# Optimization experiments

Measured on AMD Instinct MI355X. Metric: run time of the kernel, lower is better.

The kernel has to match this reference:

```python
import jax, jax.numpy as jnp
import numpy as np
from jax import lax

B, H, W, CIN = 4, 64, 64, 1024
CMID = 512
NA = 9  # 3 sizes * 3 ratios
PRE_NMS, POST_NMS, IOU_THR = 6000, 300, 0.7  # eval-mode caps (training=False)


def setup_inputs() -> dict:
    key = jax.random.key(0)
    ks = jax.random.split(key, 4)
    feats = jax.random.normal(ks[0], (B, H, W, CIN), jnp.float32)
    # anchors: normalized ccwh (cx, cy, w, h) on a stride-16 grid of a 1024px image
    stride, img = 16.0, 1024.0
    cx = (jnp.arange(W, dtype=jnp.float32) + 0.5) * stride / img
    cy = (jnp.arange(H, dtype=jnp.float32) + 0.5) * stride / img
    sizes = jnp.array([64.0, 128.0, 256.0])
    ratios = jnp.array([0.5, 1.0, 2.0])
    ws = (sizes[:, None] * jnp.sqrt(ratios)[None, :]).reshape(-1) / img  # [9]
    hs = (sizes[:, None] / jnp.sqrt(ratios)[None, :]).reshape(-1) / img  # [9]
    cyg, cxg = jnp.meshgrid(cy, cx, indexing='ij')  # [H,W]
    ancs = jnp.stack([
        jnp.broadcast_to(cxg[:, :, None], (H, W, NA)),
        jnp.broadcast_to(cyg[:, :, None], (H, W, NA)),
        jnp.broadcast_to(ws[None, None, :], (H, W, NA)),
        jnp.broadcast_to(hs[None, None, :], (H, W, NA)),
    ], axis=-1)
    ancs = jnp.broadcast_to(ancs[None], (B, H, W, NA, 4)).astype(jnp.float32)
    ancs_valid = jnp.ones((B, H, W, NA), jnp.float32)
    w_bneck = jax.random.normal(ks[1], (CIN, CMID), jnp.float32) * 0.01
    b_bneck = jnp.zeros((CMID,), jnp.float32)
    w_cls = jax.random.normal(ks[2], (CMID, NA), jnp.float32) * 0.01
    b_cls = jnp.zeros((NA,), jnp.float32)
    w_reg = jax.random.normal(ks[3], (CMID, NA * 4), jnp.float32) * 0.01
    b_reg = jnp.zeros((NA * 4,), jnp.float32)
    return dict(feats=feats, ancs=ancs, ancs_valid=ancs_valid,
                w_bneck=w_bneck, b_bneck=b_bneck, w_cls=w_cls, b_cls=b_cls,
                w_reg=w_reg, b_reg=b_reg)


def _nms(boxes, max_out, thr):
    # boxes [N,4] xyxy, sorted by score descending. Greedy NMS via lax.scan.
    x1, y1, x2, y2 = boxes[:, 0], boxes[:, 1], boxes[:, 2], boxes[:, 3]
    areas = (x2 - x1) * (y2 - y1)

    def step(valid, _):
        idx = jnp.argmax(valid)  # first still-valid box = highest score
        has = valid[idx]
        b = boxes[idx]
        a = areas[idx]
        iw = jnp.maximum(jnp.minimum(b[2], x2) - jnp.maximum(b[0], x1), 0.0)
        ih = jnp.maximum(jnp.minimum(b[3], y2) - jnp.maximum(b[1], y1), 0.0)
        inter = iw * ih
        union = a + areas - inter
        iou = jnp.where(union > 0, inter / union, 0.0)
        keep = valid & (iou <= thr)
        keep = keep.at[idx].set(False)
        return jnp.where(has, keep, valid), jnp.where(has, idx, -1)

    _, sel = lax.scan(step, jnp.ones(boxes.shape[0], bool), None, length=max_out)
    return sel  # [max_out] selected indices, -1 = no more boxes


def _forward(feats, ancs, w_bneck, b_bneck, w_cls, b_cls, w_reg, b_reg):
    h = jax.nn.relu(jnp.einsum('bhwc,cm->bhwm', feats, w_bneck) + b_bneck)
    cls_pred = jax.nn.sigmoid(jnp.einsum('bhwm,mo->bhwo', h, w_cls) + b_cls)
    reg_pred = (jnp.einsum('bhwm,mo->bhwo', h, w_reg) + b_reg).reshape(B, H, W, NA, 4)
    cls_f = cls_pred.reshape(-1)
    reg_f = reg_pred.reshape(-1, 4)
    anc_f = ancs.reshape(-1, 4)
    # apply_offsets in ccwh: cx += tx*w, cy += ty*h, w *= exp(tw), h *= exp(th)
    cx = anc_f[:, 0] + reg_f[:, 0] * anc_f[:, 2]
    cy = anc_f[:, 1] + reg_f[:, 1] * anc_f[:, 3]
    ww = anc_f[:, 2] * jnp.exp(reg_f[:, 2])
    hh = anc_f[:, 3] * jnp.exp(reg_f[:, 3])
    # ccwh -> xyxy, clip to [0,1]
    boxes = jnp.stack([cx - ww / 2, cy - hh / 2, cx + ww / 2, cy + hh / 2], axis=-1)
    boxes = jnp.clip(boxes, 0.0, 1.0)
    order = jnp.argsort(-cls_f)[:PRE_NMS]
    boxes = boxes[order]
    sel = _nms(boxes, POST_NMS, IOU_THR)
    # pad unselected slots with zeros (TF returns a variable-length tensor)
    proposals = jnp.where(sel[:, None] >= 0, boxes[jnp.clip(sel, 0)], 0.0)
    return cls_pred, reg_pred, proposals


def reference(feats, ancs, ancs_valid, w_bneck, b_bneck, w_cls, b_cls, w_reg, b_reg):
    # ancs_valid is reshaped but never used in the original extract_proposals
    return _forward(feats, ancs, w_bneck, b_bneck, w_cls, b_cls, w_reg, b_reg)
```

## Files before the change

kernel.cpp:

```cpp
#include <hip/hip_runtime.h>
#include <cstdint>
#include <cstddef>

#define P_TOT    16384
#define CIN      1024
#define CMID     512
#define NA       9
#define NANC     147456
#define PRE_NMS  6000
#define POST_NMS 300
#define IOU_THR  0.7f
#define NWORDS   94
#define NHCOPY   64

#define CLS_OFF  0
#define REG_OFF  147456
#define PROP_OFF 737280

#define WS_H        0u
#define WS_MASK     0u
#define WS_HISTN    8388608u
#define WS_LOGITS   33554432u
#define WS_BOXES    36700160u
#define WS_HIST     39059456u
#define WS_WCOMB    39059456u
#define WS_META     39321600u
#define WS_COLL     39321856u
#define WS_SBOX     39387392u
#define CAP_COLL    8192

__device__ __forceinline__ int imin(int a, int b) { return a < b ? a : b; }

__device__ __forceinline__ void gld_lds16(const float* g, float* l) {
    __builtin_amdgcn_global_load_lds(
        (const __attribute__((address_space(1))) void*)g,
        (__attribute__((address_space(3))) void*)l,
        16, 0, 0);
}

__global__ __launch_bounds__(256)
__attribute__((amdgpu_waves_per_eu(1, 2)))
void gemm1_kernel(
    const float* __restrict__ A, const float* __restrict__ Bw,
    const float* __restrict__ bias, float* __restrict__ C)
{
    __shared__ float As[2][16][132];
    __shared__ float Bs[2][16][128];

    const int t  = threadIdx.x;
    const int m0 = blockIdx.x * 128;
    const int n0 = blockIdx.y * 128;
    const int tx = t & 15;
    const int ty = t >> 4;

    const int ar0 = t >> 2;
    const int ac0 = (t & 3) * 4;

    const float* asrc0 = A + (size_t)(m0 + ar0) * CIN + ac0;
    const float* asrc1 = asrc0 + (size_t)64 * CIN;
    const float* bsrc  = Bw + (size_t)(t >> 5) * CMID + n0 + (t & 31) * 4;
    float* bdst0 = &Bs[0][0][0] + t * 4;
    float* bdst1 = &Bs[1][0][0] + t * 4;

    float4 c0a{0,0,0,0}, c0b{0,0,0,0}, c1a{0,0,0,0}, c1b{0,0,0,0};
    float4 c2a{0,0,0,0}, c2b{0,0,0,0}, c3a{0,0,0,0}, c3b{0,0,0,0};
    float4 c4a{0,0,0,0}, c4b{0,0,0,0}, c5a{0,0,0,0}, c5b{0,0,0,0};
    float4 c6a{0,0,0,0}, c6b{0,0,0,0}, c7a{0,0,0,0}, c7b{0,0,0,0};

    gld_lds16(bsrc, bdst0);
    gld_lds16(bsrc + 8 * CMID, bdst0 + 1024);
    float4 pa0 = *(const float4*)(asrc0);
    float4 pa1 = *(const float4*)(asrc1);
    As[0][ac0 + 0][ar0] = pa0.x; As[0][ac0 + 1][ar0] = pa0.y;
    As[0][ac0 + 2][ar0] = pa0.z; As[0][ac0 + 3][ar0] = pa0.w;
    As[0][ac0 + 0][ar0 + 64] = pa1.x; As[0][ac0 + 1][ar0 + 64] = pa1.y;
    As[0][ac0 + 2][ar0 + 64] = pa1.z; As[0][ac0 + 3][ar0 + 64] = pa1.w;
    __syncthreads();

#define FMA4(acc, s, b) { acc.x += (s)*(b).x; acc.y += (s)*(b).y; \
                          acc.z += (s)*(b).z; acc.w += (s)*(b).w; }

    for (int kt = 0; kt < 64; ++kt) {
        const int cur = kt & 1, nxt = cur ^ 1;
        if (kt < 63) {
            const int k0 = (kt + 1) * 16;
            float* bd = nxt ? bdst1 : bdst0;
            gld_lds16(bsrc + (size_t)k0 * CMID, bd);
            gld_lds16(bsrc + (size_t)(k0 + 8) * CMID, bd + 1024);
            pa0 = *(const float4*)(asrc0 + k0);
            pa1 = *(const float4*)(asrc1 + k0);
        }
#pragma unroll 2
        for (int kk = 0; kk < 16; ++kk) {
            float4 a0 = *(const float4*)&As[cur][kk][ty * 4];
            float4 a1 = *(const float4*)&As[cur][kk][64 + ty * 4];
            float4 b0 = *(const float4*)&Bs[cur][kk][tx * 4];
            float4 b1 = *(const float4*)&Bs[cur][kk][64 + tx * 4];
            FMA4(c0a, a0.x, b0) FMA4(c0b, a0.x, b1)
            FMA4(c1a, a0.y, b0) FMA4(c1b, a0.y, b1)
            FMA4(c2a, a0.z, b0) FMA4(c2b, a0.z, b1)
            FMA4(c3a, a0.w, b0) FMA4(c3b, a0.w, b1)
            FMA4(c4a, a1.x, b0) FMA4(c4b, a1.x, b1)
            FMA4(c5a, a1.y, b0) FMA4(c5b, a1.y, b1)
            FMA4(c6a, a1.z, b0) FMA4(c6b, a1.z, b1)
            FMA4(c7a, a1.w, b0) FMA4(c7b, a1.w, b1)
        }
        if (kt < 63) {
            As[nxt][ac0 + 0][ar0] = pa0.x; As[nxt][ac0 + 1][ar0] = pa0.y;
            As[nxt][ac0 + 2][ar0] = pa0.z; As[nxt][ac0 + 3][ar0] = pa0.w;
            As[nxt][ac0 + 0][ar0 + 64] = pa1.x; As[nxt][ac0 + 1][ar0 + 64] = pa1.y;
            As[nxt][ac0 + 2][ar0 + 64] = pa1.z; As[nxt][ac0 + 3][ar0 + 64] = pa1.w;
        }
        __syncthreads();
    }
#undef FMA4

    const float4 bias0 = *(const float4*)(bias + n0 + tx * 4);
    const float4 bias1 = *(const float4*)(bias + n0 + 64 + tx * 4);
#define STROW(row, ca, cb) { \
    float4 o; \
    o.x = fmaxf(ca.x + bias0.x, 0.f); o.y = fmaxf(ca.y + bias0.y, 0.f); \
    o.z = fmaxf(ca.z + bias0.z, 0.f); o.w = fmaxf(ca.w + bias0.w, 0.f); \
    *(float4*)(C + (size_t)(row) * CMID + n0 + tx * 4) = o; \
    o.x = fmaxf(cb.x + bias1.x, 0.f); o.y = fmaxf(cb.y + bias1.y, 0.f); \
    o.z = fmaxf(cb.z + bias1.z, 0.f); o.w = fmaxf(cb.w + bias1.w, 0.f); \
    *(float4*)(C + (size_t)(row) * CMID + n0 + 64 + tx * 4) = o; }

    const int mr = m0 + ty * 4;
    STROW(mr + 0, c0a, c0b)   STROW(mr + 1, c1a, c1b)
    STROW(mr + 2, c2a, c2b)   STROW(mr + 3, c3a, c3b)
    STROW(mr + 64, c4a, c4b)  STROW(mr + 65, c5a, c5b)
    STROW(mr + 66, c6a, c6b)  STROW(mr + 67, c7a, c7b)
#undef STROW
}

__global__ __launch_bounds__(256) void wprep_kernel(
    const float* __restrict__ wcls, const float* __restrict__ wreg,
    float* __restrict__ wcomb)
{
    int i = blockIdx.x * 256 + threadIdx.x;
    int k = i / 48, o = i - k * 48;
    float v = 0.f;
    if (o < 9)       v = wcls[k * 9 + o];
    else if (o < 45) v = wreg[k * 36 + (o - 9)];
    wcomb[i] = v;
}

__global__ __launch_bounds__(256) void gemm2_kernel(
    const float* __restrict__ h, const float* __restrict__ wcomb,
    const float* __restrict__ bcls, const float* __restrict__ breg,
    float* __restrict__ logits)
{
    __shared__ float hS[64][33];
    __shared__ float wS[32][48];

    const int t  = threadIdx.x;
    const int p0 = blockIdx.x * 64;
    const int px = t & 63;
    const int og = t >> 6;

    const int hr = t >> 2;
    const int hc = (t & 3) * 4;

    float acc[12] = {};

    for (int kt = 0; kt < 16; ++kt) {
        const int k0 = kt * 32;
        {
            const float* hp = h + (size_t)(p0 + hr) * CMID + k0 + hc;
            float4 v0 = *(const float4*)(hp);
            float4 v1 = *(const float4*)(hp + 16);
            hS[hr][hc + 0] = v0.x; hS[hr][hc + 1] = v0.y;
            hS[hr][hc + 2] = v0.z; hS[hr][hc + 3] = v0.w;
            hS[hr][16 + hc + 0] = v1.x; hS[hr][16 + hc + 1] = v1.y;
            hS[hr][16 + hc + 2] = v1.z; hS[hr][16 + hc + 3] = v1.w;
        }
        {
            int idx = t;
            if (idx < 384) {
                int kk = idx / 12, o4 = (idx - kk * 12) * 4;
                *(float4*)&wS[kk][o4] = *(const float4*)&wcomb[(size_t)(k0 + kk) * 48 + o4];
            }
            idx = t + 256;
            if (idx < 384) {
                int kk = idx / 12, o4 = (idx - kk * 12) * 4;
                *(float4*)&wS[kk][o4] = *(const float4*)&wcomb[(size_t)(k0 + kk) * 48 + o4];
            }
        }
        __syncthreads();
#pragma unroll 4
        for (int kk = 0; kk < 32; ++kk) {
            float hv = hS[px][kk];
            float4 w0 = *(const float4*)&wS[kk][og * 12];
            float4 w1 = *(const float4*)&wS[kk][og * 12 + 4];
            float4 w2 = *(const float4*)&wS[kk][og * 12 + 8];
            acc[0] += hv * w0.x; acc[1]  += hv * w0.y; acc[2]  += hv * w0.z; acc[3]  += hv * w0.w;
            acc[4] += hv * w1.x; acc[5]  += hv * w1.y; acc[6]  += hv * w1.z; acc[7]  += hv * w1.w;
            acc[8] += hv * w2.x; acc[9]  += hv * w2.y; acc[10] += hv * w2.z; acc[11] += hv * w2.w;
        }
        __syncthreads();
    }
#pragma unroll
    for (int c = 0; c < 12; ++c) {
        int o = og * 12 + c;
        if (o < 45) {
            float bv = (o < 9) ? bcls[o] : breg[o - 9];
            logits[(size_t)(p0 + px) * 48 + o] = acc[c] + bv;
        }
    }
}

__global__ __launch_bounds__(256) void decode_kernel(
    const float* __restrict__ logits, const float4* __restrict__ ancs,
    float* __restrict__ out, float4* __restrict__ boxes,
    unsigned int* __restrict__ histN)
{
    int i = blockIdx.x * 256 + threadIdx.x;
    int p = i / 9, a = i - p * 9;
    const float* lrow = logits + (size_t)p * 48;
    float lg = lrow[a];
    float score = 1.f / (1.f + expf(-lg));
    out[CLS_OFF + i] = score;

    float r0 = lrow[9 + a * 4 + 0];
    float r1 = lrow[9 + a * 4 + 1];
    float r2 = lrow[9 + a * 4 + 2];
    float r3 = lrow[9 + a * 4 + 3];
    float4 rg; rg.x = r0; rg.y = r1; rg.z = r2; rg.w = r3;
    *(float4*)(out + REG_OFF + (size_t)i * 4) = rg;

    float4 an = ancs[i];
    float cx = an.x + r0 * an.z;
    float cy = an.y + r1 * an.w;
    float ww = an.z * expf(r2);
    float hh = an.w * expf(r3);
    float4 bb;
    bb.x = fminf(fmaxf(cx - ww * 0.5f, 0.f), 1.f);
    bb.y = fminf(fmaxf(cy - hh * 0.5f, 0.f), 1.f);
    bb.z = fminf(fmaxf(cx + ww * 0.5f, 0.f), 1.f);
    bb.w = fminf(fmaxf(cy + hh * 0.5f, 0.f), 1.f);
    boxes[i] = bb;

    unsigned int sb = __float_as_uint(score);
    atomicAdd(&histN[(unsigned)(blockIdx.x & (NHCOPY - 1)) * 65536u + (sb >> 16)], 1u);
}

__global__ __launch_bounds__(256) void hreduce_kernel(
    const unsigned int* __restrict__ histN, unsigned int* __restrict__ hist)
{
    int b = blockIdx.x * 256 + threadIdx.x;
    unsigned int s = 0;
#pragma unroll 8
    for (int c = 0; c < NHCOPY; ++c) s += histN[(unsigned)c * 65536u + b];
    hist[b] = s;
}

__global__ __launch_bounds__(256) void scan_kernel(
    const unsigned int* __restrict__ hist, unsigned int* __restrict__ meta)
{
    __shared__ unsigned int sums[256];
    __shared__ unsigned int sc[256];
    __shared__ unsigned int sc2[256];
    __shared__ int cstar;
    __shared__ unsigned int saShared;
    __shared__ int tbin;

    int t = threadIdx.x;
    if (t == 0) tbin = -1;

    unsigned int s = 0;
    int base = t << 8;
    for (int b = 0; b < 256; b += 4) {
        uint4 v = *(const uint4*)(hist + base + b);
        s += v.x + v.y + v.z + v.w;
    }
    sums[t] = s;
    __syncthreads();

    sc[t] = sums[255 - t];
    __syncthreads();
    for (int off = 1; off < 256; off <<= 1) {
        unsigned int v = sc[t];
        unsigned int add = (t >= off) ? sc[t - off] : 0u;
        __syncthreads();
        sc[t] = v + add;
        __syncthreads();
    }
    {
        unsigned int sa = (t == 255) ? 0u : sc[254 - t];
        if (sa < PRE_NMS && sa + sums[t] >= PRE_NMS) { cstar = t; saShared = sa; }
    }
    __syncthreads();

    int c = cstar;
    unsigned int SA = saShared;
    sc2[t] = hist[c * 256 + 255 - t];
    __syncthreads();
    for (int off = 1; off < 256; off <<= 1) {
        unsigned int v = sc2[t];
        unsigned int add = (t >= off) ? sc2[t - off] : 0u;
        __syncthreads();
        sc2[t] = v + add;
        __syncthreads();
    }
    {
        unsigned int si = sc2[255 - t];
        int cand = (SA + si >= PRE_NMS) ? t : -1;
        atomicMax(&tbin, cand);
    }
    __syncthreads();
    if (t == 0) meta[1] = (unsigned int)(c * 256 + tbin);
}

__global__ __launch_bounds__(256) void collect_kernel(
    const float* __restrict__ scores, const unsigned int* __restrict__ meta,
    unsigned long long* __restrict__ coll, unsigned int* __restrict__ cnt)
{
    int i = blockIdx.x * 256 + threadIdx.x;
    unsigned int T = meta[1];
    unsigned int sb = __float_as_uint(scores[i]);
    if ((sb >> 16) >= T) {
        unsigned int pos = atomicAdd(cnt, 1u);
        if (pos < CAP_COLL)
            coll[pos] = ((unsigned long long)sb << 32) |
                        (unsigned long long)(0xFFFFFFFFu - (unsigned int)i);
    }
}

__global__ __launch_bounds__(256) void rank_kernel(
    const unsigned long long* __restrict__ coll,
    const unsigned int* __restrict__ cnt,
    const float4* __restrict__ boxes, float4* __restrict__ sboxes)
{
    const int t = threadIdx.x;
    const int lane = t & 63;
    const int gwave = blockIdx.x * 4 + (t >> 6);
    unsigned int n = cnt[0];
    if (n > CAP_COLL) n = CAP_COLL;
    if (gwave * 16 >= (int)n) return;

    unsigned long long me[16];
    int rank[16];
#pragma unroll
    for (int i = 0; i < 16; ++i) {
        int mi = gwave * 16 + i;
        me[i] = (mi < (int)n) ? coll[mi] : ~0ULL;
        rank[i] = 0;
    }

    for (int j = 0; j < CAP_COLL; j += 64) {
        unsigned long long k = ((unsigned)(j + lane) < n) ? coll[j + lane] : 0ULL;
#pragma unroll
        for (int i = 0; i < 16; ++i)
            rank[i] += (int)__popcll(__ballot(k > me[i]));
    }

#pragma unroll
    for (int i = 0; i < 16; ++i) {
        int mi = gwave * 16 + i;
        if (mi < (int)n && rank[i] < PRE_NMS && lane == i) {
            unsigned int idx = 0xFFFFFFFFu - (unsigned int)(me[i] & 0xFFFFFFFFULL);
            if (idx > NANC - 1) idx = NANC - 1;
            sboxes[rank[i]] = boxes[idx];
        }
    }
}

__global__ __launch_bounds__(64) void nmsmat_kernel(
    const float4* __restrict__ sboxes, unsigned long long* __restrict__ mask)
{
    const int rb = blockIdx.x, cb = blockIdx.y;
    if (cb < rb) return;
    __shared__ float cx1[64], cy1[64], cx2[64], cy2[64], car[64];

    const int t = threadIdx.x;
    const int c = cb * 64 + t;
    float4 b = (c < PRE_NMS) ? sboxes[c] : make_float4(0.f, 0.f, 0.f, 0.f);
    cx1[t] = b.x; cy1[t] = b.y; cx2[t] = b.z; cy2[t] = b.w;
    car[t] = (b.z - b.x) * (b.w - b.y);
    __syncthreads();

    const int r = rb * 64 + t;
    if (r >= PRE_NMS) return;
    const float4 rbx = sboxes[r];
    const float ra = (rbx.z - rbx.x) * (rbx.w - rbx.y);

    unsigned long long w = 0ULL;
#pragma unroll 8
    for (int i = 0; i < 64; ++i) {
        int j = cb * 64 + i;
        float iw = fmaxf(fminf(rbx.z, cx2[i]) - fmaxf(rbx.x, cx1[i]), 0.f);
        float ih = fmaxf(fminf(rbx.w, cy2[i]) - fmaxf(rbx.y, cy1[i]), 0.f);
        float inter = iw * ih;
        float uni = ra + car[i] - inter;
        float iou = (uni > 0.f) ? (inter / uni) : 0.f;
        if (iou > IOU_THR && j > r) w |= (1ULL << i);
    }
    mask[(size_t)r * NWORDS + cb] = w;
}

__global__ __launch_bounds__(64) void nmsresolve_kernel(
    const float4* __restrict__ sboxes,
    const unsigned long long* __restrict__ mask,
    float* __restrict__ prop)
{
    const int t = threadIdx.x;
    for (int j = t; j < POST_NMS * 4; j += 64) prop[j] = 0.f;

    const int w0 = 2 * t, w1 = 2 * t + 1;
    unsigned long long v0 = 0ULL, v1 = 0ULL;
    if (w0 < 93) v0 = ~0ULL; else if (w0 == 93) v0 = (1ULL << 48) - 1ULL;
    if (w1 < 93) v1 = ~0ULL; else if (w1 == 93) v1 = (1ULL << 48) - 1ULL;

    int cnt = 0;
    while (cnt < POST_NMS) {
        int c = 0x7fffffff;
        if (v0) c = (w0 << 6) + __builtin_ctzll(v0);
        else if (v1) c = (w1 << 6) + __builtin_ctzll(v1);
        unsigned long long bal = __ballot((v0 | v1) != 0ULL);
        if (!bal) break;
        int F = __builtin_ctzll(bal);
        int g = __shfl(c, F, 64);
        const int wg = g >> 6, bg = g & 63;

        if (t == 0) {
            float4 bb = sboxes[g];
            *(float4*)(prop + cnt * 4) = bb;
        }
        unsigned long long mx = 0ULL, my = 0ULL;
        if (t < 47) {
            const ulonglong2* row2 = (const ulonglong2*)(mask + (size_t)g * NWORDS);
            ulonglong2 mm = row2[t];
            mx = mm.x; my = mm.y;
        }
        unsigned long long m0 = (w0 >= wg) ? mx : 0ULL;
        unsigned long long m1 = (w1 >= wg) ? my : 0ULL;
        v0 &= ~m0; v1 &= ~m1;
        if (w0 == wg) v0 &= ~(1ULL << bg);
        if (w1 == wg) v1 &= ~(1ULL << bg);
        ++cnt;
    }
}

extern "C" void kernel_launch(void* const* d_in, const int* in_sizes, int n_in,
                              void* d_out, int out_size, void* d_ws, size_t ws_size,
                              hipStream_t stream)
{
    const float*  feats   = (const float*)d_in[0];
    const float4* ancs    = (const float4*)d_in[1];
    const float*  w_bneck = (const float*)d_in[3];
    const float*  b_bneck = (const float*)d_in[4];
    const float*  w_cls   = (const float*)d_in[5];
    const float*  b_cls   = (const float*)d_in[6];
    const float*  w_reg   = (const float*)d_in[7];
    const float*  b_reg   = (const float*)d_in[8];

    float* out = (float*)d_out;
    char*  ws  = (char*)d_ws;
    float*              h      = (float*)(ws + WS_H);
    float*              logits = (float*)(ws + WS_LOGITS);
    float4*             boxes  = (float4*)(ws + WS_BOXES);
    unsigned int*       histN  = (unsigned int*)(ws + WS_HISTN);
    unsigned int*       hist   = (unsigned int*)(ws + WS_HIST);
    float*              wcomb  = (float*)(ws + WS_WCOMB);
    unsigned int*       meta   = (unsigned int*)(ws + WS_META);
    unsigned long long* coll   = (unsigned long long*)(ws + WS_COLL);
    float4*             sboxes = (float4*)(ws + WS_SBOX);
    unsigned long long* mask   = (unsigned long long*)(ws + WS_MASK);

    hipMemsetAsync(ws + WS_META, 0, 256, stream);

    wprep_kernel<<<96, 256, 0, stream>>>(w_cls, w_reg, wcomb);
    gemm1_kernel<<<dim3(128, 4), 256, 0, stream>>>(feats, w_bneck, b_bneck, h);
    gemm2_kernel<<<256, 256, 0, stream>>>(h, wcomb, b_cls, b_reg, logits);
    hipMemsetAsync(ws + WS_HISTN, 0, (size_t)NHCOPY * 65536 * 4, stream);
    decode_kernel<<<576, 256, 0, stream>>>(logits, ancs, out, boxes, histN);
    hreduce_kernel<<<256, 256, 0, stream>>>(histN, hist);
    scan_kernel<<<1, 256, 0, stream>>>(hist, meta);
    collect_kernel<<<576, 256, 0, stream>>>(out, meta, coll, &meta[0]);
    rank_kernel<<<128, 256, 0, stream>>>(coll, meta, boxes, sboxes);
    nmsmat_kernel<<<dim3(94, 94), 64, 0, stream>>>(sboxes, mask);
    nmsresolve_kernel<<<1, 64, 0, stream>>>(sboxes, mask, out + PROP_OFF);
}
```

Before: 648.7 us.

## Fold weight prep into gemm1, read B from global, batch NMS resolve

gemm1 no longer stages the weight tile through LDS and reads B rows straight from global memory inside the inner loop. The separate wprep kernel is folded into gemm1's first block, and the meta memset is replaced by resetting meta[0] inside the scan kernel. The serial NMS resolve loop now picks up to 8 candidates per round and prefetches their mask rows before applying them in order, to hide global-load latency. The aim is fewer launches and less serial latency. The cost is possibly worse GEMM memory behaviour and a reliance on meta fields other than meta[0] not needing a zero reset.

```diff
diff --git a/kernel.cpp b/kernel.cpp
--- a/kernel.cpp
+++ b/kernel.cpp
@@ -31,21 +31,25 @@
 
 __device__ __forceinline__ int imin(int a, int b) { return a < b ? a : b; }
 
-__device__ __forceinline__ void gld_lds16(const float* g, float* l) {
-    __builtin_amdgcn_global_load_lds(
-        (const __attribute__((address_space(1))) void*)g,
-        (__attribute__((address_space(3))) void*)l,
-        16, 0, 0);
-}
-
 __global__ __launch_bounds__(256)
 __attribute__((amdgpu_waves_per_eu(1, 2)))
 void gemm1_kernel(
     const float* __restrict__ A, const float* __restrict__ Bw,
-    const float* __restrict__ bias, float* __restrict__ C)
-{
+    const float* __restrict__ bias, float* __restrict__ C,
+    const float* __restrict__ wcls, const float* __restrict__ wreg,
+    float* __restrict__ wcomb)
+{
+    if (blockIdx.x == 0 && blockIdx.y == 0) {
+        for (int i = threadIdx.x; i < 24576; i += 256) {
+            int k = i / 48, o = i - k * 48;
+            float v = 0.f;
+            if (o < 9)       v = wcls[k * 9 + o];
+            else if (o < 45) v = wreg[k * 36 + (o - 9)];
+            wcomb[i] = v;
+        }
+    }
+
     __shared__ float As[2][16][132];
-    __shared__ float Bs[2][16][128];
 
     const int t  = threadIdx.x;
     const int m0 = blockIdx.x * 128;
@@ -58,17 +62,13 @@
 
     const float* asrc0 = A + (size_t)(m0 + ar0) * CIN + ac0;
     const float* asrc1 = asrc0 + (size_t)64 * CIN;
-    const float* bsrc  = Bw + (size_t)(t >> 5) * CMID + n0 + (t & 31) * 4;
-    float* bdst0 = &Bs[0][0][0] + t * 4;
-    float* bdst1 = &Bs[1][0][0] + t * 4;
+    const float* bbase = Bw + n0 + tx * 4;
 
     float4 c0a{0,0,0,0}, c0b{0,0,0,0}, c1a{0,0,0,0}, c1b{0,0,0,0};
     float4 c2a{0,0,0,0}, c2b{0,0,0,0}, c3a{0,0,0,0}, c3b{0,0,0,0};
     float4 c4a{0,0,0,0}, c4b{0,0,0,0}, c5a{0,0,0,0}, c5b{0,0,0,0};
     float4 c6a{0,0,0,0}, c6b{0,0,0,0}, c7a{0,0,0,0}, c7b{0,0,0,0};
 
-    gld_lds16(bsrc, bdst0);
-    gld_lds16(bsrc + 8 * CMID, bdst0 + 1024);
     float4 pa0 = *(const float4*)(asrc0);
     float4 pa1 = *(const float4*)(asrc1);
     As[0][ac0 + 0][ar0] = pa0.x; As[0][ac0 + 1][ar0] = pa0.y;
@@ -84,18 +84,17 @@
         const int cur = kt & 1, nxt = cur ^ 1;
         if (kt < 63) {
             const int k0 = (kt + 1) * 16;
-            float* bd = nxt ? bdst1 : bdst0;
-            gld_lds16(bsrc + (size_t)k0 * CMID, bd);
-            gld_lds16(bsrc + (size_t)(k0 + 8) * CMID, bd + 1024);
             pa0 = *(const float4*)(asrc0 + k0);
             pa1 = *(const float4*)(asrc1 + k0);
         }
+        const float* brow = bbase + (size_t)(kt * 16) * CMID;
 #pragma unroll 2
         for (int kk = 0; kk < 16; ++kk) {
+            float4 b0 = *(const float4*)(brow);
+            float4 b1 = *(const float4*)(brow + 64);
+            brow += CMID;
             float4 a0 = *(const float4*)&As[cur][kk][ty * 4];
             float4 a1 = *(const float4*)&As[cur][kk][64 + ty * 4];
-            float4 b0 = *(const float4*)&Bs[cur][kk][tx * 4];
-            float4 b1 = *(const float4*)&Bs[cur][kk][64 + tx * 4];
             FMA4(c0a, a0.x, b0) FMA4(c0b, a0.x, b1)
             FMA4(c1a, a0.y, b0) FMA4(c1b, a0.y, b1)
             FMA4(c2a, a0.z, b0) FMA4(c2b, a0.z, b1)
@@ -132,18 +131,6 @@
     STROW(mr + 64, c4a, c4b)  STROW(mr + 65, c5a, c5b)
     STROW(mr + 66, c6a, c6b)  STROW(mr + 67, c7a, c7b)
 #undef STROW
-}
-
-__global__ __launch_bounds__(256) void wprep_kernel(
-    const float* __restrict__ wcls, const float* __restrict__ wreg,
-    float* __restrict__ wcomb)
-{
-    int i = blockIdx.x * 256 + threadIdx.x;
-    int k = i / 48, o = i - k * 48;
-    float v = 0.f;
-    if (o < 9)       v = wcls[k * 9 + o];
-    else if (o < 45) v = wreg[k * 36 + (o - 9)];
-    wcomb[i] = v;
 }
 
 __global__ __launch_bounds__(256) void gemm2_kernel(
@@ -309,7 +296,7 @@
         atomicMax(&tbin, cand);
     }
     __syncthreads();
-    if (t == 0) meta[1] = (unsigned int)(c * 256 + tbin);
+    if (t == 0) { meta[1] = (unsigned int)(c * 256 + tbin); meta[0] = 0u; }
 }
 
 __global__ __launch_bounds__(256) void collect_kernel(
@@ -414,31 +401,57 @@
 
     int cnt = 0;
     while (cnt < POST_NMS) {
-        int c = 0x7fffffff;
-        if (v0) c = (w0 << 6) + __builtin_ctzll(v0);
-        else if (v1) c = (w1 << 6) + __builtin_ctzll(v1);
-        unsigned long long bal = __ballot((v0 | v1) != 0ULL);
-        if (!bal) break;
-        int F = __builtin_ctzll(bal);
-        int g = __shfl(c, F, 64);
-        const int wg = g >> 6, bg = g & 63;
-
-        if (t == 0) {
-            float4 bb = sboxes[g];
-            *(float4*)(prop + cnt * 4) = bb;
-        }
-        unsigned long long mx = 0ULL, my = 0ULL;
-        if (t < 47) {
-            const ulonglong2* row2 = (const ulonglong2*)(mask + (size_t)g * NWORDS);
-            ulonglong2 mm = row2[t];
-            mx = mm.x; my = mm.y;
-        }
-        unsigned long long m0 = (w0 >= wg) ? mx : 0ULL;
-        unsigned long long m1 = (w1 >= wg) ? my : 0ULL;
-        v0 &= ~m0; v1 &= ~m1;
-        if (w0 == wg) v0 &= ~(1ULL << bg);
-        if (w1 == wg) v1 &= ~(1ULL << bg);
-        ++cnt;
+        unsigned long long s0 = v0, s1 = v1;
+        int gs[8];
+#pragma unroll
+        for (int q = 0; q < 8; ++q) {
+            int c = 0x7fffffff;
+            if (s0) c = (w0 << 6) + __builtin_ctzll(s0);
+            else if (s1) c = (w1 << 6) + __builtin_ctzll(s1);
+            unsigned long long bal = __ballot((s0 | s1) != 0ULL);
+            int g = -1;
+            if (bal) {
+                int F = __builtin_ctzll(bal);
+                g = __shfl(c, F, 64);
+                int wq = g >> 6;
+                unsigned long long bit = 1ULL << (g & 63);
+                if (w0 == wq) s0 &= ~bit;
+                if (w1 == wq) s1 &= ~bit;
+            }
+            gs[q] = g;
+        }
+        if (gs[0] < 0) break;
+
+        unsigned long long rx[8], ry[8];
+#pragma unroll
+        for (int q = 0; q < 8; ++q) {
+            rx[q] = 0ULL; ry[q] = 0ULL;
+            if (gs[q] >= 0 && t < 47) {
+                const ulonglong2* row2 = (const ulonglong2*)(mask + (size_t)gs[q] * NWORDS);
+                ulonglong2 mm = row2[t];
+                rx[q] = mm.x; ry[q] = mm.y;
+            }
+        }
+
+#pragma unroll
+        for (int q = 0; q < 8; ++q) {
+            int g = gs[q];
+            if (g >= 0 && cnt < POST_NMS) {
+                int wq = g >> 6;
+                unsigned long long bit = 1ULL << (g & 63);
+                bool aliveLane = (w0 == wq && (v0 & bit)) || (w1 == wq && (v1 & bit));
+                unsigned long long ab = __ballot(aliveLane);
+                if (ab) {
+                    if (t == 0) *(float4*)(prop + cnt * 4) = sboxes[g];
+                    unsigned long long m0 = (w0 >= wq) ? rx[q] : 0ULL;
+                    unsigned long long m1 = (w1 >= wq) ? ry[q] : 0ULL;
+                    v0 &= ~m0; v1 &= ~m1;
+                    if (w0 == wq) v0 &= ~bit;
+                    if (w1 == wq) v1 &= ~bit;
+                    ++cnt;
+                }
+            }
+        }
     }
 }
 
@@ -468,10 +481,8 @@
     float4*             sboxes = (float4*)(ws + WS_SBOX);
     unsigned long long* mask   = (unsigned long long*)(ws + WS_MASK);
 
-    hipMemsetAsync(ws + WS_META, 0, 256, stream);
-
-    wprep_kernel<<<96, 256, 0, stream>>>(w_cls, w_reg, wcomb);
-    gemm1_kernel<<<dim3(128, 4), 256, 0, stream>>>(feats, w_bneck, b_bneck, h);
+    gemm1_kernel<<<dim3(128, 4), 256, 0, stream>>>(feats, w_bneck, b_bneck, h,
+                                                   w_cls, w_reg, wcomb);
     gemm2_kernel<<<256, 256, 0, stream>>>(h, wcomb, b_cls, b_reg, logits);
     hipMemsetAsync(ws + WS_HISTN, 0, (size_t)NHCOPY * 65536 * 4, stream);
     decode_kernel<<<576, 256, 0, stream>>>(logits, ancs, out, boxes, histN);
```

Result: slower. 703.2 us (+8.4%).
